# Performance work log

Measured on AMD Instinct MI355X. Metric: run time of the kernel, lower is better.

Reference implementation:

```python
import jax, jax.numpy as jnp
import numpy as np

EPS = 1e-12

def _l2norm(v, axis=-1):
    # F.normalize with eps=1e-12
    n = jnp.sqrt(jnp.sum(v * v, axis=axis, keepdims=True))
    return v / jnp.maximum(n, EPS)

def setup_inputs() -> dict:
    key = jax.random.key(0)
    k1, k2, k3, k4, k5 = jax.random.split(key, 5)
    B, N, D_IN, D_OUT, S, P = 8, 1024, 384, 384, 128, 128
    x = jax.random.normal(k1, (B, N, D_IN), dtype=jnp.float32)
    pos_embed = jax.random.normal(k2, (N, P), dtype=jnp.float32)
    maps_weight = jax.random.normal(k3, (S, P), dtype=jnp.float32) * 0.02
    scale = jnp.ones((), dtype=jnp.float32)
    weight = jax.random.normal(k4, (D_OUT, D_IN, S), dtype=jnp.float32) * 0.02
    bias = jax.random.normal(k5, (D_OUT, S), dtype=jnp.float32) * 0.02
    return {"x": x, "pos_embed": pos_embed, "maps_weight": maps_weight,
            "scale": scale, "weight": weight, "bias": bias}

def reference(x, pos_embed, maps_weight, scale, weight, bias):
    # TopoMaps (token_wise=False): softmax over slots
    pe = _l2norm(pos_embed)                 # (N, P)
    w = scale * _l2norm(maps_weight)        # (S, P)
    coef = jax.nn.softmax(pe @ w.T, axis=-1)  # (N, S)
    # Combine expert weights per token: (N, out, in)
    W = jnp.einsum('ns,dcs->ndc', coef, weight)
    b = coef @ bias.T                        # (N, out)
    out = jnp.einsum('bnc,ndc->bnd', x, W) + b
    return out
```

## Files before the change

kernel.cpp:

```cpp
#include <hip/hip_runtime.h>
#include <hip/hip_bf16.h>

#define EPSN 1e-12f

#define BB   8
#define NN   1024
#define DIN  384
#define DOUT 384
#define SS   128
#define PP   128

#define NCQ  97

typedef __attribute__((ext_vector_type(8))) short bf16x8;
typedef __attribute__((ext_vector_type(4))) float f32x4;

__device__ __forceinline__ float bf2f(unsigned short u) {
    union { unsigned int i; float f; } v; v.i = ((unsigned int)u) << 16; return v.f;
}

__global__ void wnorm_kernel(const float* __restrict__ mw,
                             const float* __restrict__ scale,
                             float* __restrict__ wnT) {
    __shared__ float row[PP];
    const int s = blockIdx.x, t = threadIdx.x;
    row[t] = mw[s * PP + t];
    __syncthreads();
    float ss = 0.f;
#pragma unroll
    for (int p = 0; p < PP; ++p) ss = fmaf(row[p], row[p], ss);
    wnT[t * SS + s] = scale[0] * row[t] / fmaxf(sqrtf(ss), EPSN);
}

__global__ void coef_kernel(const float* __restrict__ pe,
                            const float* __restrict__ wnT,
                            __hip_bfloat16* __restrict__ coefbf) {
    __shared__ float pen[PP];
    __shared__ float red[SS];
    const int n = blockIdx.x, t = threadIdx.x;
    pen[t] = pe[n * PP + t];
    __syncthreads();
    float ss = 0.f;
#pragma unroll
    for (int p = 0; p < PP; ++p) ss = fmaf(pen[p], pen[p], ss);
    const float rn = 1.0f / fmaxf(sqrtf(ss), EPSN);
    float lg = 0.f;
#pragma unroll
    for (int p = 0; p < PP; ++p) lg = fmaf(pen[p], wnT[p * SS + t], lg);
    lg *= rn;
    red[t] = lg;
    __syncthreads();
    for (int off = 64; off > 0; off >>= 1) {
        if (t < off) red[t] = fmaxf(red[t], red[t + off]);
        __syncthreads();
    }
    const float m = red[0];
    __syncthreads();
    const float e = expf(lg - m);
    red[t] = e;
    __syncthreads();
    for (int off = 64; off > 0; off >>= 1) {
        if (t < off) red[t] += red[t + off];
        __syncthreads();
    }
    coefbf[n * SS + t] = __float2bfloat16(e / red[0]);
}

__global__ void wfrag_prep(const float* __restrict__ weight,
                           const float* __restrict__ bias,
                           __hip_bfloat16* __restrict__ wfrag) {
    const int id = blockIdx.x * 256 + threadIdx.x;
    const int lane = id & 63;
    const int kt = (id >> 6) & 3;
    const int rem = id >> 8;
    const int cq = rem % NCQ;
    const int dblk = rem / NCQ;
    const int l15 = lane & 15, g = lane >> 4;
    const int d = dblk * 4 + (l15 & 3);
    const int s0 = kt * 32 + g * 8;
    __hip_bfloat16* dst = wfrag + (size_t)id * 8;
    if (cq < 96) {
        const int c = cq * 4 + (l15 >> 2);
        const float* src = weight + ((size_t)d * DIN + c) * SS + s0;
#pragma unroll
        for (int j = 0; j < 8; ++j) dst[j] = __float2bfloat16(src[j]);
    } else if ((l15 >> 2) == 0) {
        const float* src = bias + (size_t)d * SS + s0;
#pragma unroll
        for (int j = 0; j < 8; ++j) dst[j] = __float2bfloat16(src[j]);
    } else {
#pragma unroll
        for (int j = 0; j < 8; ++j) dst[j] = __float2bfloat16(0.f);
    }
}

__global__ void xfrag_prep(const float* __restrict__ x,
                           __hip_bfloat16* __restrict__ xfrag) {
    const int id = blockIdx.x * 256 + threadIdx.x;
    const int n = id / 388, cc = id % 388;
    const int ngrp = n >> 6, nhalf = (n >> 5) & 1, nt = (n >> 4) & 1, l15 = n & 15;
    const int cq = cc >> 2, g = cc & 3;
    const size_t G = (((size_t)ngrp * 2 + nhalf) * NCQ + cq) * 2 + nt;
    __hip_bfloat16* dst = xfrag + (G * 64 + (g * 16 + l15)) * 8;
    if (cc < 384) {
#pragma unroll
        for (int b = 0; b < BB; ++b)
            dst[b] = __float2bfloat16(x[((size_t)b * NN + n) * DIN + cc]);
    } else {
        const __hip_bfloat16 v = __float2bfloat16(cc == 384 ? 1.0f : 0.0f);
#pragma unroll
        for (int b = 0; b < BB; ++b) dst[b] = v;
    }
}

__global__ __launch_bounds__(128, 3) void topo_mfma_kernel(
    const __hip_bfloat16* __restrict__ wfrag,
    const __hip_bfloat16* __restrict__ xfrag,
    const __hip_bfloat16* __restrict__ coefbf,
    float* __restrict__ out) {
    const int tid   = threadIdx.x;
    const int lane  = tid & 63;
    const int nhalf = tid >> 6;
    const int l15   = lane & 15;
    const int g     = lane >> 4;

    const int bid  = blockIdx.x;
    const int xcd  = bid & 7;
    const int slot = bid >> 3;
    const int dgrp = xcd * 12 + (slot >> 4);
    const int ngrp = slot & 15;

    bf16x8 cf[2][4];
#pragma unroll
    for (int nt = 0; nt < 2; ++nt) {
        const int n = ngrp * 64 + nhalf * 32 + nt * 16 + l15;
#pragma unroll
        for (int kt = 0; kt < 4; ++kt)
            cf[nt][kt] = *reinterpret_cast<const bf16x8*>(coefbf + n * SS + kt * 32 + g * 8);
    }

    f32x4 acc[2][BB];
#pragma unroll
    for (int nt = 0; nt < 2; ++nt)
#pragma unroll
        for (int b = 0; b < BB; ++b) acc[nt][b] = (f32x4){0.f, 0.f, 0.f, 0.f};

    const size_t xgbase = ((size_t)ngrp * 2 + nhalf) * NCQ;
    const bf16x8* abase = reinterpret_cast<const bf16x8*>(wfrag) +
                          ((size_t)dgrp * NCQ * 4) * 64 + lane;

    for (int cq = 0; cq < NCQ; ++cq) {
        bf16x8 xf[2];
#pragma unroll
        for (int nt = 0; nt < 2; ++nt)
            xf[nt] = *reinterpret_cast<const bf16x8*>(
                xfrag + (((xgbase + cq) * 2 + nt) * 64 + lane) * 8);

        const bf16x8* ab = abase + (size_t)cq * 4 * 64;
        const bf16x8 af0 = ab[0];
        const bf16x8 af1 = ab[64];
        const bf16x8 af2 = ab[128];
        const bf16x8 af3 = ab[192];

#pragma unroll
        for (int nt = 0; nt < 2; ++nt) {
            f32x4 wq = (f32x4){0.f, 0.f, 0.f, 0.f};
            wq = __builtin_amdgcn_mfma_f32_16x16x32_bf16(af0, cf[nt][0], wq, 0, 0, 0);
            wq = __builtin_amdgcn_mfma_f32_16x16x32_bf16(af1, cf[nt][1], wq, 0, 0, 0);
            wq = __builtin_amdgcn_mfma_f32_16x16x32_bf16(af2, cf[nt][2], wq, 0, 0, 0);
            wq = __builtin_amdgcn_mfma_f32_16x16x32_bf16(af3, cf[nt][3], wq, 0, 0, 0);
#pragma unroll
            for (int b = 0; b < BB; ++b) {
                const float xb = bf2f((unsigned short)xf[nt][b]);
                acc[nt][b] += wq * xb;
            }
        }
    }

#pragma unroll
    for (int nt = 0; nt < 2; ++nt) {
        const int n = ngrp * 64 + nhalf * 32 + nt * 16 + l15;
        const int dbase = dgrp * 4;
#pragma unroll
        for (int b = 0; b < BB; ++b) {
            f32x4 a = acc[nt][b];
#pragma unroll
            for (int r = 0; r < 4; ++r) {
                float v = a[r];
                v += __shfl_xor(v, 16);
                v += __shfl_xor(v, 32);
                a[r] = v;
            }
            if ((b >> 1) == g) {
                *reinterpret_cast<f32x4*>(out + ((size_t)b * NN + n) * DOUT + dbase) = a;
            }
        }
    }
}

extern "C" void kernel_launch(void* const* d_in, const int* in_sizes, int n_in,
                              void* d_out, int out_size, void* d_ws, size_t ws_size,
                              hipStream_t stream) {
    const float* x     = (const float*)d_in[0];
    const float* pe    = (const float*)d_in[1];
    const float* mw    = (const float*)d_in[2];
    const float* scale = (const float*)d_in[3];
    const float* wgt   = (const float*)d_in[4];
    const float* bias  = (const float*)d_in[5];
    float* out = (float*)d_out;

    char* ws = (char*)d_ws;
    float*          wnT    = (float*)(ws + 0);
    __hip_bfloat16* coefbf = (__hip_bfloat16*)(ws + 65536);
    __hip_bfloat16* xfrag  = (__hip_bfloat16*)(ws + 327680);
    __hip_bfloat16* wfrag  = (__hip_bfloat16*)(ws + 6684672);

    wnorm_kernel<<<dim3(SS), dim3(PP), 0, stream>>>(mw, scale, wnT);
    coef_kernel<<<dim3(NN), dim3(PP), 0, stream>>>(pe, wnT, coefbf);
    xfrag_prep<<<dim3((NN * 388) / 256), dim3(256), 0, stream>>>(x, xfrag);
    wfrag_prep<<<dim3((96 * NCQ * 4 * 64) / 256), dim3(256), 0, stream>>>(wgt, bias, wfrag);
    topo_mfma_kernel<<<dim3(1536), dim3(128), 0, stream>>>(wfrag, xfrag, coefbf, out);
}
```

Measured before the change: 225.3 us.

## Stage weight fragments in double-buffered LDS shared by four waves per block

Doubles the block to four waves covering 128 tokens. The weight fragments for a d-group are loaded once per block into a double-buffered LDS staging area with global_load_lds, and prefetched four cq steps ahead. Before, each wave read them directly from global memory, so the aim is to cut redundant global and L2 weight traffic and hide load latency. The cost is per-chunk block barriers, 32KB of LDS per block (which may limit occupancy), and half as many blocks.

```diff
diff --git a/kernel.cpp b/kernel.cpp
--- a/kernel.cpp
+++ b/kernel.cpp
@@ -18,6 +18,11 @@
 __device__ __forceinline__ float bf2f(unsigned short u) {
     union { unsigned int i; float f; } v; v.i = ((unsigned int)u) << 16; return v.f;
 }
+
+#define GLOAD_LDS(gp, lp)                                                            \
+    __builtin_amdgcn_global_load_lds(                                                \
+        (const __attribute__((address_space(1))) unsigned int*)(gp),                 \
+        (__attribute__((address_space(3))) unsigned int*)(lp), 16, 0, 0)
 
 __global__ void wnorm_kernel(const float* __restrict__ mw,
                              const float* __restrict__ scale,
@@ -98,9 +103,9 @@
                            __hip_bfloat16* __restrict__ xfrag) {
     const int id = blockIdx.x * 256 + threadIdx.x;
     const int n = id / 388, cc = id % 388;
-    const int ngrp = n >> 6, nhalf = (n >> 5) & 1, nt = (n >> 4) & 1, l15 = n & 15;
+    const int tg = n >> 5, nt = (n >> 4) & 1, l15 = n & 15;
     const int cq = cc >> 2, g = cc & 3;
-    const size_t G = (((size_t)ngrp * 2 + nhalf) * NCQ + cq) * 2 + nt;
+    const size_t G = ((size_t)tg * NCQ + cq) * 2 + nt;
     __hip_bfloat16* dst = xfrag + (G * 64 + (g * 16 + l15)) * 8;
     if (cc < 384) {
 #pragma unroll
@@ -113,27 +118,29 @@
     }
 }
 
-__global__ __launch_bounds__(128, 3) void topo_mfma_kernel(
+__global__ __launch_bounds__(256, 3) void topo_mfma_kernel(
     const __hip_bfloat16* __restrict__ wfrag,
     const __hip_bfloat16* __restrict__ xfrag,
     const __hip_bfloat16* __restrict__ coefbf,
     float* __restrict__ out) {
-    const int tid   = threadIdx.x;
-    const int lane  = tid & 63;
-    const int nhalf = tid >> 6;
-    const int l15   = lane & 15;
-    const int g     = lane >> 4;
+    __shared__ __align__(16) char sbuf[2][16384];
+
+    const int tid  = threadIdx.x;
+    const int lane = tid & 63;
+    const int wq   = tid >> 6;
+    const int l15  = lane & 15;
+    const int g    = lane >> 4;
 
     const int bid  = blockIdx.x;
     const int xcd  = bid & 7;
     const int slot = bid >> 3;
-    const int dgrp = xcd * 12 + (slot >> 4);
-    const int ngrp = slot & 15;
+    const int dgrp = xcd * 12 + (slot >> 3);
+    const int ngrp = slot & 7;
 
     bf16x8 cf[2][4];
 #pragma unroll
     for (int nt = 0; nt < 2; ++nt) {
-        const int n = ngrp * 64 + nhalf * 32 + nt * 16 + l15;
+        const int n = ngrp * 128 + wq * 32 + nt * 16 + l15;
 #pragma unroll
         for (int kt = 0; kt < 4; ++kt)
             cf[nt][kt] = *reinterpret_cast<const bf16x8*>(coefbf + n * SS + kt * 32 + g * 8);
@@ -145,41 +152,69 @@
 #pragma unroll
         for (int b = 0; b < BB; ++b) acc[nt][b] = (f32x4){0.f, 0.f, 0.f, 0.f};
 
-    const size_t xgbase = ((size_t)ngrp * 2 + nhalf) * NCQ;
-    const bf16x8* abase = reinterpret_cast<const bf16x8*>(wfrag) +
-                          ((size_t)dgrp * NCQ * 4) * 64 + lane;
-
-    for (int cq = 0; cq < NCQ; ++cq) {
-        bf16x8 xf[2];
-#pragma unroll
-        for (int nt = 0; nt < 2; ++nt)
-            xf[nt] = *reinterpret_cast<const bf16x8*>(
-                xfrag + (((xgbase + cq) * 2 + nt) * 64 + lane) * 8);
-
-        const bf16x8* ab = abase + (size_t)cq * 4 * 64;
-        const bf16x8 af0 = ab[0];
-        const bf16x8 af1 = ab[64];
-        const bf16x8 af2 = ab[128];
-        const bf16x8 af3 = ab[192];
-
-#pragma unroll
-        for (int nt = 0; nt < 2; ++nt) {
-            f32x4 wq = (f32x4){0.f, 0.f, 0.f, 0.f};
-            wq = __builtin_amdgcn_mfma_f32_16x16x32_bf16(af0, cf[nt][0], wq, 0, 0, 0);
-            wq = __builtin_amdgcn_mfma_f32_16x16x32_bf16(af1, cf[nt][1], wq, 0, 0, 0);
-            wq = __builtin_amdgcn_mfma_f32_16x16x32_bf16(af2, cf[nt][2], wq, 0, 0, 0);
-            wq = __builtin_amdgcn_mfma_f32_16x16x32_bf16(af3, cf[nt][3], wq, 0, 0, 0);
-#pragma unroll
-            for (int b = 0; b < BB; ++b) {
-                const float xb = bf2f((unsigned short)xf[nt][b]);
-                acc[nt][b] += wq * xb;
+    const int tg = ngrp * 4 + wq;
+    const size_t xgbase = (size_t)tg * NCQ;
+    const char* wsrc = (const char*)wfrag + (size_t)dgrp * NCQ * 4096;
+
+#pragma unroll
+    for (int k = 0; k < 4; ++k)
+        GLOAD_LDS(wsrc + ((size_t)k * 256 + wq * 64 + lane) * 16,
+                  sbuf[0] + ((size_t)k * 256 + wq * 64) * 16);
+    __syncthreads();
+
+    int par = 0;
+    for (int ci = 0; ci < 25; ++ci) {
+        const int cq0 = ci * 4;
+        const int ncq = (ci == 24) ? 1 : 4;
+
+        if (ci < 24) {
+            const int nnext = (ci == 23) ? 1 : 4;
+            const char* src = wsrc + (size_t)(cq0 + 4) * 4096;
+            char* dst = sbuf[par ^ 1];
+#pragma unroll
+            for (int k = 0; k < 4; ++k)
+                if (k < nnext)
+                    GLOAD_LDS(src + ((size_t)k * 256 + wq * 64 + lane) * 16,
+                              dst + ((size_t)k * 256 + wq * 64) * 16);
+        }
+
+        for (int cqs = 0; cqs < ncq; ++cqs) {
+            const int cq = cq0 + cqs;
+            bf16x8 xf[2];
+#pragma unroll
+            for (int nt = 0; nt < 2; ++nt)
+                xf[nt] = *reinterpret_cast<const bf16x8*>(
+                    xfrag + (((xgbase + cq) * 2 + nt) * 64 + lane) * 8);
+
+            const bf16x8* afp =
+                reinterpret_cast<const bf16x8*>(sbuf[par] + (size_t)cqs * 4096) + lane;
+            const bf16x8 af0 = afp[0];
+            const bf16x8 af1 = afp[64];
+            const bf16x8 af2 = afp[128];
+            const bf16x8 af3 = afp[192];
+
+#pragma unroll
+            for (int nt = 0; nt < 2; ++nt) {
+                f32x4 wq4 = (f32x4){0.f, 0.f, 0.f, 0.f};
+                wq4 = __builtin_amdgcn_mfma_f32_16x16x32_bf16(af0, cf[nt][0], wq4, 0, 0, 0);
+                wq4 = __builtin_amdgcn_mfma_f32_16x16x32_bf16(af1, cf[nt][1], wq4, 0, 0, 0);
+                wq4 = __builtin_amdgcn_mfma_f32_16x16x32_bf16(af2, cf[nt][2], wq4, 0, 0, 0);
+                wq4 = __builtin_amdgcn_mfma_f32_16x16x32_bf16(af3, cf[nt][3], wq4, 0, 0, 0);
+#pragma unroll
+                for (int b = 0; b < BB; ++b) {
+                    const float xb = bf2f((unsigned short)xf[nt][b]);
+                    acc[nt][b] += wq4 * xb;
+                }
             }
         }
+
+        __syncthreads();
+        par ^= 1;
     }
 
 #pragma unroll
     for (int nt = 0; nt < 2; ++nt) {
-        const int n = ngrp * 64 + nhalf * 32 + nt * 16 + l15;
+        const int n = ngrp * 128 + wq * 32 + nt * 16 + l15;
         const int dbase = dgrp * 4;
 #pragma unroll
         for (int b = 0; b < BB; ++b) {
@@ -219,5 +254,5 @@
     coef_kernel<<<dim3(NN), dim3(PP), 0, stream>>>(pe, wnT, coefbf);
     xfrag_prep<<<dim3((NN * 388) / 256), dim3(256), 0, stream>>>(x, xfrag);
     wfrag_prep<<<dim3((96 * NCQ * 4 * 64) / 256), dim3(256), 0, stream>>>(wgt, bias, wfrag);
-    topo_mfma_kernel<<<dim3(1536), dim3(128), 0, stream>>>(wfrag, xfrag, coefbf, out);
-}
+    topo_mfma_kernel<<<dim3(768), dim3(256), 0, stream>>>(wfrag, xfrag, coefbf, out);
+}
```

New measurement: 222.6 us. About the same (-1.2%).
